# Kernel tuning notes

Hardware: AMD Instinct MI355X
Metric: run time of the kernel (lower is better)

## Reference

```python
import jax, jax.numpy as jnp
import numpy as np

B = 8192          # batch_size = len(embedds)
D = 512           # ll_p['num_channels'][-1]
C = 100           # n_classes
N_LAB = 4096      # int(B * plb), plb = 0.5
MAX_ITER = 30     # gtg_i
TOL = 1e-3        # gtg_t
ENT_EPS = 1e-20


def _mlp(x, W1, b1, W2, b2, W3, b3, Wc, bc):
    h = jax.nn.relu(x @ W1 + b1)
    h = jax.nn.relu(h @ W2 + b2)
    h = jax.nn.relu(h @ W3 + b3)
    return (h @ Wc + bc)[:, 0]  # squeeze -> [B]


def _entropy(X):
    # per-row Shannon entropy (bits), as in ALGTG utils
    return -jnp.sum(X * jnp.log2(X + ENT_EPS), axis=1)


def _gtg_entropy_hist(embedds, labels):
    # get_A: cos_sim -> zero diagonal -> clamp [0,1] -> 'mean' threshold -> 'diversity' (1-A)
    n = jnp.maximum(jnp.linalg.norm(embedds, axis=-1, keepdims=True), 1e-12)
    E = embedds / n
    A = E @ E.T                                   # [B,B]
    A = A * (1.0 - jnp.eye(B, dtype=A.dtype))     # fill_diagonal_(0)
    A = jnp.clip(A, 0.0, 1.0)
    A = jnp.where(A < jnp.mean(A), 0.0, A)        # AM_threshold_strategy == 'mean'
    A = 1.0 - A                                   # AM_strategy == 'diversity'

    # get_X: labeled rows one-hot, unlabeled rows uniform 1/C
    lab = jnp.arange(B) < N_LAB
    X0 = jnp.where(lab[:, None],
                   jax.nn.one_hot(labels, C, dtype=jnp.float32),
                   jnp.full((B, C), 1.0 / C, jnp.float32))
    hist0 = jnp.zeros((B, MAX_ITER), jnp.float32)
    unlab = ~lab

    def cond(s):
        _X, _h, i, err = s
        return (err > TOL) & (i < MAX_ITER)

    def body(s):
        X, hist, i, _err = s
        Xn = X * (A @ X)                          # replicator dynamics step
        Xn = Xn / jnp.sum(Xn, axis=1, keepdims=True)
        ent = _entropy(Xn)
        hist = hist.at[:, i].set(jnp.where(unlab, ent, 0.0))
        return (Xn, hist, i + 1, jnp.linalg.norm(Xn - X))

    init = (X0, hist0, jnp.array(0, jnp.int32), jnp.array(jnp.inf, jnp.float32))
    _, hist, _, _ = jax.lax.while_loop(cond, body, init)
    return hist


def setup_inputs() -> dict:
    key = jax.random.key(0)
    ks = jax.random.split(key, 11)
    d2, d4, d8 = D // 2, D // 4, D // 8

    def lin(k, fi, fo):
        return jax.random.normal(k, (fi, fo), jnp.float32) / np.float32(np.sqrt(fi))

    return {
        'features': jax.random.normal(ks[0], (B, 64), jnp.float32),
        'embedds': jax.random.normal(ks[1], (B, D), jnp.float32),
        'labels': jax.random.randint(ks[2], (B,), 0, C),
        'W1': lin(ks[3], D, d2), 'b1': jnp.zeros((d2,), jnp.float32),
        'W2': lin(ks[4], d2, d4), 'b2': jnp.zeros((d4,), jnp.float32),
        'W3': lin(ks[5], d4, d8), 'b3': jnp.zeros((d8,), jnp.float32),
        'Wc': lin(ks[6], d8, 1), 'bc': jnp.zeros((1,), jnp.float32),
    }


def reference(features, embedds, labels, W1, b1, W2, b2, W3, b3, Wc, bc):
    y_pred = _mlp(embedds, W1, b1, W2, b2, W3, b3, Wc, bc)        # [B]
    hist = _gtg_entropy_hist(embedds, labels)                      # [B, MAX_ITER]
    y_true = jnp.mean(hist, axis=1)                                # ent_strategy == 'mean'
    labeled_mask = jnp.arange(B) < N_LAB                           # bool [B]
    return (y_pred, y_true, labeled_mask)
```

## Files before the change

kernel.cpp:

```cpp
#include <hip/hip_runtime.h>
#include <hip/hip_bf16.h>
#include <math.h>

namespace {
constexpr int BROWS = 8192;
constexpr int NLAB  = 4096;
constexpr int NUNL  = 4096;
constexpr int CREAL = 100;
constexpr int CPAD  = 112;
constexpr int DIM   = 512;
constexpr int MAXIT = 30;

constexpr size_t MiB = 1ull << 20;
constexpr size_t OFF_S    = 0;
constexpr size_t OFF_AU   = 64 * MiB;
constexpr size_t OFF_EB   = 96 * MiB;
constexpr size_t OFF_XT0  = 96 * MiB;
constexpr size_t OFF_XT1  = 98 * MiB;
constexpr size_t OFF_XU   = 100 * MiB;
constexpr size_t OFF_PL   = 102 * MiB;
constexpr size_t OFF_HIST = 104 * MiB;
constexpr size_t OFF_ERR  = 104 * MiB + 16384;
constexpr size_t OFF_MS   = 104 * MiB + 16768;
constexpr size_t OFF_RN   = 104 * MiB + 32768;
constexpr size_t MEMSET_LEN = 20480;
}

typedef __attribute__((ext_vector_type(8))) short short8;
typedef __attribute__((ext_vector_type(4))) float floatx4;

__device__ inline ushort f2bf(float f) {
  __hip_bfloat16 h = __float2bfloat16(f);
  union { __hip_bfloat16 b; ushort u; } c; c.b = h; return c.u;
}
__device__ inline float bf2f(ushort u) {
  union { ushort u; __hip_bfloat16 b; } c; c.u = u;
  return __bfloat162float(c.b);
}
__device__ inline short8 ntload_s8(const ushort* p) {
  return __builtin_nontemporal_load((const short8*)p);
}

__global__ __launch_bounds__(64) void k_prep(const float* __restrict__ emb,
                                             ushort* __restrict__ Eb,
                                             float* __restrict__ rn) {
  int row = blockIdx.x, l = threadIdx.x;
  const float4* e4 = (const float4*)(emb + (size_t)row * DIM);
  float4 a = e4[2 * l], b = e4[2 * l + 1];
  float f[8] = {a.x, a.y, a.z, a.w, b.x, b.y, b.z, b.w};
  float s = 0.f;
#pragma unroll
  for (int q = 0; q < 8; q++) s += f[q] * f[q];
#pragma unroll
  for (int m = 1; m < 64; m <<= 1) s += __shfl_xor(s, m);
  if (l == 0) rn[row] = 1.0f / fmaxf(sqrtf(s), 1e-12f);
  union { short8 v; ushort u[8]; } o;
#pragma unroll
  for (int q = 0; q < 8; q++) o.u[q] = f2bf(f[q]);
  *(short8*)(Eb + (size_t)row * DIM + l * 8) = o.v;
}

__global__ __launch_bounds__(256) void k_initX(ushort* __restrict__ X0,
                                               ushort* __restrict__ X1,
                                               float* __restrict__ Xu,
                                               const int* __restrict__ labels) {
  int j = blockIdx.x * 256 + threadIdx.x;
  int c = blockIdx.y;
  float v;
  if (j < NLAB) v = (labels[j] == c) ? 1.0f : 0.0f;
  else          v = (c < CREAL) ? 0.01f : 0.0f;
  ushort b = f2bf(v);
  X0[(size_t)c * BROWS + j] = b;
  X1[(size_t)c * BROWS + j] = b;
  if (j >= NLAB) Xu[(size_t)(j - NLAB) * CPAD + c] = (c < CREAL) ? 0.01f : 0.0f;
}

__global__ __launch_bounds__(256) void k_mlp(const float* __restrict__ emb,
                                             const float* __restrict__ W1, const float* __restrict__ b1,
                                             const float* __restrict__ W2, const float* __restrict__ b2,
                                             const float* __restrict__ W3, const float* __restrict__ b3,
                                             const float* __restrict__ Wc, const float* __restrict__ bc,
                                             float* __restrict__ out) {
  __shared__ float xs[4][512];
  __shared__ float h1[4][256];
  __shared__ float h2[4][128];
  __shared__ float h3[4][64];
  int t = threadIdx.x;
  int r0 = blockIdx.x * 4;
  {
    const float4* src = (const float4*)(emb + (size_t)r0 * DIM);
    float4* dst = (float4*)&xs[0][0];
    dst[t] = src[t];
    dst[t + 256] = src[t + 256];
  }
  __syncthreads();
  {
    float a0 = 0.f, a1 = 0.f, a2 = 0.f, a3 = 0.f;
    for (int k = 0; k < 512; k++) {
      float w = W1[k * 256 + t];
      a0 = fmaf(xs[0][k], w, a0);
      a1 = fmaf(xs[1][k], w, a1);
      a2 = fmaf(xs[2][k], w, a2);
      a3 = fmaf(xs[3][k], w, a3);
    }
    float bb = b1[t];
    h1[0][t] = fmaxf(a0 + bb, 0.f);
    h1[1][t] = fmaxf(a1 + bb, 0.f);
    h1[2][t] = fmaxf(a2 + bb, 0.f);
    h1[3][t] = fmaxf(a3 + bb, 0.f);
  }
  __syncthreads();
  {
    int c = t & 127, rb = (t >> 7) * 2;
    float a0 = 0.f, a1 = 0.f;
    for (int k = 0; k < 256; k++) {
      float w = W2[k * 128 + c];
      a0 = fmaf(h1[rb][k], w, a0);
      a1 = fmaf(h1[rb + 1][k], w, a1);
    }
    float bb = b2[c];
    h2[rb][c] = fmaxf(a0 + bb, 0.f);
    h2[rb + 1][c] = fmaxf(a1 + bb, 0.f);
  }
  __syncthreads();
  {
    int c = t & 63, r = t >> 6;
    float a = 0.f;
    for (int k = 0; k < 128; k++) a = fmaf(h2[r][k], W3[k * 64 + c], a);
    h3[r][c] = fmaxf(a + b3[c], 0.f);
  }
  __syncthreads();
  {
    int r = t >> 6, l = t & 63;
    float v = h3[r][l] * Wc[l];
#pragma unroll
    for (int m = 32; m; m >>= 1) v += __shfl_down(v, m);
    if (l == 0) out[r0 + r] = v + bc[0];
  }
}

__global__ __launch_bounds__(256) void k_simM(const ushort* __restrict__ Eb,
                                              const float* __restrict__ rn,
                                              ushort* __restrict__ S,
                                              double* __restrict__ meansum) {
  int x = blockIdx.x, y = blockIdx.y;
  if (x < 32 && y > x) return;
  __shared__ ushort Ei[128 * 40];
  __shared__ ushort Ej[128 * 40];
  __shared__ float redbuf[4];

  int t = threadIdx.x;
  int w = t >> 6, lane = t & 63;
  int m = lane & 15, g = lane >> 4;
  int ib = (w >> 1) * 64, jb = (w & 1) * 64;
  int i0 = x * 128, j0 = y * 128;

  floatx4 acc[4][4];
#pragma unroll
  for (int a = 0; a < 4; a++)
#pragma unroll
    for (int b = 0; b < 4; b++) acc[a][b] = (floatx4)0.0f;

  int lrow = t >> 1, lhalf = (t & 1) * 16;
  for (int kt = 0; kt < DIM; kt += 32) {
    __syncthreads();
    {
      const ushort* gi = Eb + (size_t)(i0 + lrow) * DIM + kt + lhalf;
      const ushort* gj = Eb + (size_t)(j0 + lrow) * DIM + kt + lhalf;
      int o = lrow * 40 + lhalf;
      *(short8*)&Ei[o]     = *(const short8*)gi;
      *(short8*)&Ei[o + 8] = *(const short8*)(gi + 8);
      *(short8*)&Ej[o]     = *(const short8*)gj;
      *(short8*)&Ej[o + 8] = *(const short8*)(gj + 8);
    }
    __syncthreads();

    short8 ah[4], bh[4];
#pragma unroll
    for (int rt = 0; rt < 4; rt++) ah[rt] = *(const short8*)&Ei[(ib + rt * 16 + m) * 40 + g * 8];
#pragma unroll
    for (int ct = 0; ct < 4; ct++) bh[ct] = *(const short8*)&Ej[(jb + ct * 16 + m) * 40 + g * 8];
#pragma unroll
    for (int rt = 0; rt < 4; rt++)
#pragma unroll
      for (int ct = 0; ct < 4; ct++)
        acc[rt][ct] = __builtin_amdgcn_mfma_f32_16x16x32_bf16(ah[rt], bh[ct], acc[rt][ct], 0, 0, 0);
  }

  bool dostore = (x >= 32);
  bool isdiag  = (x == y);
  float weight = (x < 32) ? (isdiag ? 1.0f : 2.0f) : ((y < 32) ? 2.0f : 1.0f);
  float lsum = 0.f;
#pragma unroll
  for (int rt = 0; rt < 4; rt++) {
    int gi0 = i0 + ib + rt * 16 + g * 4;
    float4 rni = *(const float4*)(rn + gi0);
#pragma unroll
    for (int ct = 0; ct < 4; ct++) {
      int gj = j0 + jb + ct * 16 + m;
      float rnj = rn[gj];
#pragma unroll
      for (int r = 0; r < 4; r++) {
        int gi = gi0 + r;
        float rv = (r == 0) ? rni.x : (r == 1) ? rni.y : (r == 2) ? rni.z : rni.w;
        float s = acc[rt][ct][r] * rv * rnj;
        if (isdiag && gi == gj) s = 0.f;
        s = fminf(fmaxf(s, 0.f), 1.f);
        lsum += s;
        if (dostore) S[(size_t)(gi - NLAB) * BROWS + gj] = f2bf(s);
      }
    }
  }
  lsum *= weight;
#pragma unroll
  for (int d = 1; d < 64; d <<= 1) lsum += __shfl_xor(lsum, d);
  if (lane == 0) redbuf[w] = lsum;
  __syncthreads();
  if (t == 0) atomicAdd(meansum, (double)(redbuf[0] + redbuf[1] + redbuf[2] + redbuf[3]));
}

__global__ __launch_bounds__(1024, 4) void k_iter(const ushort* __restrict__ S,
                                                  ushort* __restrict__ Au,
                                                  const ushort* __restrict__ XTr,
                                                  ushort* __restrict__ XTw,
                                                  float* __restrict__ Xu,
                                                  float* __restrict__ Plab,
                                                  float* __restrict__ hist,
                                                  float* __restrict__ errsq,
                                                  const double* __restrict__ ms,
                                                  int it) {
  if (it > 0 && errsq[it - 1] <= 1e-6f) return;
  __shared__ float part[8][16 * 113];
  __shared__ float Pbuf[16 * 114];
  __shared__ float dsqbuf[16];
  ushort* xbuf = (ushort*)&part[0][0];
  int t = threadIdx.x;
  int w = t >> 6, lane = t & 63;
  int m = lane & 15, g = lane >> 4;
  int r0 = blockIdx.x * 16;

  float2 xo = make_float2(0.f, 0.f);
  if (lane < 56) xo = *(const float2*)(Xu + (size_t)(r0 + w) * CPAD + lane * 2);
  float pl_pre[2] = {0.f, 0.f};
  if (it > 0) {
#pragma unroll
    for (int q = 0; q < 2; q++) {
      int idx = t + q * 1024;
      if (idx < 16 * CPAD)
        pl_pre[q] = Plab[(size_t)(r0 + idx / CPAD) * CPAD + idx % CPAD];
    }
  }

  floatx4 acc[7];
#pragma unroll
  for (int c = 0; c < 7; c++) acc[c] = (floatx4)0.0f;

  if (it == 0) {
    float mean = (float)(ms[0] * (1.0 / ((double)BROWS * (double)BROWS)));
    int kw = w * 512;
    for (int ks = 0; ks < 16; ks++) {
      int kk = kw + ks * 32;
      size_t so = (size_t)(r0 + m) * BROWS + kk + g * 8;
      short8 a = ntload_s8(S + so);
      union { short8 v; ushort u[8]; } ua; ua.v = a;
#pragma unroll
      for (int e = 0; e < 8; e++) {
        float s = bf2f(ua.u[e]);
        float av = (s < mean) ? 1.0f : 1.0f - s;
        ua.u[e] = f2bf(av);
      }
      a = ua.v;
      if (w >= 8)
        *(short8*)(Au + (size_t)(r0 + m) * NUNL + (kk - NLAB) + g * 8) = a;
#pragma unroll
      for (int ct = 0; ct < 7; ct++) {
        short8 b = *(const short8*)(XTr + (size_t)(ct * 16 + m) * BROWS + kk + g * 8);
        acc[ct] = __builtin_amdgcn_mfma_f32_16x16x32_bf16(a, b, acc[ct], 0, 0, 0);
      }
    }
  } else {
    int kw = w * 256;
    size_t abase = (size_t)(r0 + m) * NUNL + kw + g * 8;
    size_t bbase = (size_t)m * BROWS + NLAB + kw + g * 8;
    for (int ks = 0; ks < 8; ks++) {
      short8 a = ntload_s8(Au + abase + ks * 32);
#pragma unroll
      for (int ct = 0; ct < 7; ct++) {
        short8 b = *(const short8*)(XTr + bbase + (size_t)ct * 16 * BROWS + ks * 32);
        acc[ct] = __builtin_amdgcn_mfma_f32_16x16x32_bf16(a, b, acc[ct], 0, 0, 0);
      }
    }
  }

  if (w < 8) {
#pragma unroll
    for (int ct = 0; ct < 7; ct++)
#pragma unroll
      for (int r = 0; r < 4; r++)
        part[w][(g * 4 + r) * 113 + ct * 16 + m] = acc[ct][r];
  }
  __syncthreads();
  float sA[2] = {0.f, 0.f}, sB[2] = {0.f, 0.f};
#pragma unroll
  for (int q = 0; q < 2; q++) {
    int idx = t + q * 1024;
    if (idx < 16 * CPAD) {
      int row = idx / CPAD, col = idx % CPAD;
      int o = row * 113 + col;
      sA[q] = ((part[0][o] + part[1][o]) + (part[2][o] + part[3][o]))
            + ((part[4][o] + part[5][o]) + (part[6][o] + part[7][o]));
    }
  }
  __syncthreads();
  if (w >= 8) {
#pragma unroll
    for (int ct = 0; ct < 7; ct++)
#pragma unroll
      for (int r = 0; r < 4; r++)
        part[w - 8][(g * 4 + r) * 113 + ct * 16 + m] = acc[ct][r];
  }
  __syncthreads();
#pragma unroll
  for (int q = 0; q < 2; q++) {
    int idx = t + q * 1024;
    if (idx < 16 * CPAD) {
      int row = idx / CPAD, col = idx % CPAD;
      int o = row * 113 + col;
      sB[q] = ((part[0][o] + part[1][o]) + (part[2][o] + part[3][o]))
            + ((part[4][o] + part[5][o]) + (part[6][o] + part[7][o]));
      float P;
      size_t go = (size_t)(r0 + row) * CPAD + col;
      if (it == 0) { Plab[go] = sA[q]; P = sA[q] + sB[q]; }
      else         { P = sA[q] + sB[q] + pl_pre[q]; }
      Pbuf[row * 114 + col] = P;
    }
  }
  __syncthreads();

  int gr = r0 + w;
  bool act = lane < 56;
  float2 p = make_float2(0.f, 0.f);
  if (act) p = *(const float2*)&Pbuf[w * 114 + lane * 2];
  float2 xn;
  xn.x = xo.x * p.x;
  xn.y = xo.y * p.y;
  float s = xn.x + xn.y;
#pragma unroll
  for (int d = 1; d < 64; d <<= 1) s += __shfl_xor(s, d);
  float inv = 1.0f / s;
  float ent = 0.f, dsq = 0.f;
  if (act) {
    xn.x *= inv; xn.y *= inv;
    ent = -(xn.x * log2f(xn.x + 1e-20f) + xn.y * log2f(xn.y + 1e-20f));
    float dx = xn.x - xo.x, dy = xn.y - xo.y;
    dsq = dx * dx + dy * dy;
    *(float2*)(Xu + (size_t)gr * CPAD + lane * 2) = xn;
    int c0 = lane * 2;
    xbuf[c0 * 18 + w]       = f2bf(xn.x);
    xbuf[(c0 + 1) * 18 + w] = f2bf(xn.y);
  }
#pragma unroll
  for (int d = 1; d < 64; d <<= 1) { ent += __shfl_xor(ent, d); dsq += __shfl_xor(dsq, d); }
  if (lane == 0) {
    hist[gr] += ent;
    dsqbuf[w] = dsq;
  }
  __syncthreads();

  if (t < CPAD * 8) {
    int c = t >> 3, jl = (t & 7) * 2;
    ushort2 v = *(const ushort2*)&xbuf[c * 18 + jl];
    *(ushort2*)(XTw + (size_t)c * BROWS + NLAB + r0 + jl) = v;
  }
  if (t == 0) {
    float ds = 0.f;
#pragma unroll
    for (int i = 0; i < 16; i++) ds += dsqbuf[i];
    atomicAdd(&errsq[it], ds);
  }
}

__global__ __launch_bounds__(256) void k_final(const float* __restrict__ hist,
                                               float* __restrict__ out) {
  int i = blockIdx.x * 256 + threadIdx.x;
  float yt = (i < NLAB) ? 0.0f : hist[i - NLAB] * (1.0f / 30.0f);
  out[BROWS + i] = yt;
  out[2 * BROWS + i] = (i < NLAB) ? 1.0f : 0.0f;
}

extern "C" void kernel_launch(void* const* d_in, const int* in_sizes, int n_in,
                              void* d_out, int out_size, void* d_ws, size_t ws_size,
                              hipStream_t stream) {
  const float* emb    = (const float*)d_in[1];
  const int*   labels = (const int*)d_in[2];
  const float* W1 = (const float*)d_in[3];
  const float* b1 = (const float*)d_in[4];
  const float* W2 = (const float*)d_in[5];
  const float* b2 = (const float*)d_in[6];
  const float* W3 = (const float*)d_in[7];
  const float* b3 = (const float*)d_in[8];
  const float* Wc = (const float*)d_in[9];
  const float* bc = (const float*)d_in[10];
  float* out = (float*)d_out;

  char* ws = (char*)d_ws;
  ushort* S    = (ushort*)(ws + OFF_S);
  ushort* Au   = (ushort*)(ws + OFF_AU);
  ushort* Eb   = (ushort*)(ws + OFF_EB);
  ushort* XT0  = (ushort*)(ws + OFF_XT0);
  ushort* XT1  = (ushort*)(ws + OFF_XT1);
  float*  Xu   = (float*)(ws + OFF_XU);
  float*  Plab = (float*)(ws + OFF_PL);
  float*  hist = (float*)(ws + OFF_HIST);
  float*  errs = (float*)(ws + OFF_ERR);
  double* ms   = (double*)(ws + OFF_MS);
  float*  rn   = (float*)(ws + OFF_RN);

  hipMemsetAsync(ws + OFF_HIST, 0, MEMSET_LEN, stream);

  k_prep<<<BROWS, 64, 0, stream>>>(emb, Eb, rn);
  k_mlp<<<BROWS / 4, 256, 0, stream>>>(emb, W1, b1, W2, b2, W3, b3, Wc, bc, out);

  { dim3 g(BROWS / 128, BROWS / 128); k_simM<<<g, 256, 0, stream>>>(Eb, rn, S, ms); }

  { dim3 g(BROWS / 256, CPAD); k_initX<<<g, 256, 0, stream>>>(XT0, XT1, Xu, labels); }

  for (int it = 0; it < MAXIT; it++) {
    const ushort* XTr = (it & 1) ? XT1 : XT0;
    ushort*       XTw = (it & 1) ? XT0 : XT1;
    k_iter<<<NUNL / 16, 1024, 0, stream>>>(S, Au, XTr, XTw, Xu, Plab, hist, errs, ms, it);
  }

  k_final<<<BROWS / 256, 256, 0, stream>>>(hist, out);
}
```

Measured before the change: 779.4 us.

## Batch 8 rows per MLP block, swizzle simM LDS, drop nontemporal loads

The MLP kernel now processes 8 rows per block instead of 4, so each weight load is reused across twice as many rows. The similarity GEMM kernel XOR-swizzles its shared-memory tile columns to reduce LDS bank conflicts on the MFMA operand reads. The iteration kernel replaces nontemporal loads of S and Au with ordinary loads, which may let the Au matrix that is reread every iteration stay in cache. Risks are higher LDS use and register pressure in the MLP, and cache pollution from the S stream.

```diff
diff --git a/kernel.cpp b/kernel.cpp
--- a/kernel.cpp
+++ b/kernel.cpp
@@ -37,9 +37,6 @@
   union { ushort u; __hip_bfloat16 b; } c; c.u = u;
   return __bfloat162float(c.b);
 }
-__device__ inline short8 ntload_s8(const ushort* p) {
-  return __builtin_nontemporal_load((const short8*)p);
-}
 
 __global__ __launch_bounds__(64) void k_prep(const float* __restrict__ emb,
                                              ushort* __restrict__ Eb,
@@ -81,61 +78,70 @@
                                              const float* __restrict__ W3, const float* __restrict__ b3,
                                              const float* __restrict__ Wc, const float* __restrict__ bc,
                                              float* __restrict__ out) {
-  __shared__ float xs[4][512];
-  __shared__ float h1[4][256];
-  __shared__ float h2[4][128];
-  __shared__ float h3[4][64];
+  __shared__ float xs[8][512];
+  __shared__ float h1[8][256];
+  __shared__ float h2[8][128];
+  __shared__ float h3[8][64];
   int t = threadIdx.x;
-  int r0 = blockIdx.x * 4;
+  int r0 = blockIdx.x * 8;
   {
     const float4* src = (const float4*)(emb + (size_t)r0 * DIM);
     float4* dst = (float4*)&xs[0][0];
-    dst[t] = src[t];
-    dst[t + 256] = src[t + 256];
+#pragma unroll
+    for (int q = 0; q < 4; q++) dst[t + q * 256] = src[t + q * 256];
   }
   __syncthreads();
   {
-    float a0 = 0.f, a1 = 0.f, a2 = 0.f, a3 = 0.f;
+    float a[8];
+#pragma unroll
+    for (int r = 0; r < 8; r++) a[r] = 0.f;
     for (int k = 0; k < 512; k++) {
-      float w = W1[k * 256 + t];
-      a0 = fmaf(xs[0][k], w, a0);
-      a1 = fmaf(xs[1][k], w, a1);
-      a2 = fmaf(xs[2][k], w, a2);
-      a3 = fmaf(xs[3][k], w, a3);
+      float wv = W1[k * 256 + t];
+#pragma unroll
+      for (int r = 0; r < 8; r++) a[r] = fmaf(xs[r][k], wv, a[r]);
     }
     float bb = b1[t];
-    h1[0][t] = fmaxf(a0 + bb, 0.f);
-    h1[1][t] = fmaxf(a1 + bb, 0.f);
-    h1[2][t] = fmaxf(a2 + bb, 0.f);
-    h1[3][t] = fmaxf(a3 + bb, 0.f);
+#pragma unroll
+    for (int r = 0; r < 8; r++) h1[r][t] = fmaxf(a[r] + bb, 0.f);
   }
   __syncthreads();
   {
-    int c = t & 127, rb = (t >> 7) * 2;
+    int c = t & 127, rb = (t >> 7) * 4;
+    float a[4];
+#pragma unroll
+    for (int r = 0; r < 4; r++) a[r] = 0.f;
+    for (int k = 0; k < 256; k++) {
+      float wv = W2[k * 128 + c];
+#pragma unroll
+      for (int r = 0; r < 4; r++) a[r] = fmaf(h1[rb + r][k], wv, a[r]);
+    }
+    float bb = b2[c];
+#pragma unroll
+    for (int r = 0; r < 4; r++) h2[rb + r][c] = fmaxf(a[r] + bb, 0.f);
+  }
+  __syncthreads();
+  {
+    int c = t & 63, rb = (t >> 6) * 2;
     float a0 = 0.f, a1 = 0.f;
-    for (int k = 0; k < 256; k++) {
-      float w = W2[k * 128 + c];
-      a0 = fmaf(h1[rb][k], w, a0);
-      a1 = fmaf(h1[rb + 1][k], w, a1);
-    }
-    float bb = b2[c];
-    h2[rb][c] = fmaxf(a0 + bb, 0.f);
-    h2[rb + 1][c] = fmaxf(a1 + bb, 0.f);
+    for (int k = 0; k < 128; k++) {
+      float wv = W3[k * 64 + c];
+      a0 = fmaf(h2[rb][k], wv, a0);
+      a1 = fmaf(h2[rb + 1][k], wv, a1);
+    }
+    h3[rb][c]     = fmaxf(a0 + b3[c], 0.f);
+    h3[rb + 1][c] = fmaxf(a1 + b3[c], 0.f);
   }
   __syncthreads();
   {
-    int c = t & 63, r = t >> 6;
-    float a = 0.f;
-    for (int k = 0; k < 128; k++) a = fmaf(h2[r][k], W3[k * 64 + c], a);
-    h3[r][c] = fmaxf(a + b3[c], 0.f);
-  }
-  __syncthreads();
-  {
-    int r = t >> 6, l = t & 63;
-    float v = h3[r][l] * Wc[l];
-#pragma unroll
-    for (int m = 32; m; m >>= 1) v += __shfl_down(v, m);
-    if (l == 0) out[r0 + r] = v + bc[0];
+    int w = t >> 6, l = t & 63;
+#pragma unroll
+    for (int rr = 0; rr < 2; rr++) {
+      int r = w * 2 + rr;
+      float v = h3[r][l] * Wc[l];
+#pragma unroll
+      for (int mm = 32; mm; mm >>= 1) v += __shfl_down(v, mm);
+      if (l == 0) out[r0 + r] = v + bc[0];
+    }
   }
 }
 
@@ -162,24 +168,34 @@
     for (int b = 0; b < 4; b++) acc[a][b] = (floatx4)0.0f;
 
   int lrow = t >> 1, lhalf = (t & 1) * 16;
+  int swz = ((lrow >> 3) & 3) << 3;
+  int sb  = lrow * 40;
+  int sc0 = lhalf ^ swz, sc1 = (lhalf + 8) ^ swz;
   for (int kt = 0; kt < DIM; kt += 32) {
     __syncthreads();
     {
       const ushort* gi = Eb + (size_t)(i0 + lrow) * DIM + kt + lhalf;
       const ushort* gj = Eb + (size_t)(j0 + lrow) * DIM + kt + lhalf;
-      int o = lrow * 40 + lhalf;
-      *(short8*)&Ei[o]     = *(const short8*)gi;
-      *(short8*)&Ei[o + 8] = *(const short8*)(gi + 8);
-      *(short8*)&Ej[o]     = *(const short8*)gj;
-      *(short8*)&Ej[o + 8] = *(const short8*)(gj + 8);
+      *(short8*)&Ei[sb + sc0] = *(const short8*)gi;
+      *(short8*)&Ei[sb + sc1] = *(const short8*)(gi + 8);
+      *(short8*)&Ej[sb + sc0] = *(const short8*)gj;
+      *(short8*)&Ej[sb + sc1] = *(const short8*)(gj + 8);
     }
     __syncthreads();
 
     short8 ah[4], bh[4];
 #pragma unroll
-    for (int rt = 0; rt < 4; rt++) ah[rt] = *(const short8*)&Ei[(ib + rt * 16 + m) * 40 + g * 8];
-#pragma unroll
-    for (int ct = 0; ct < 4; ct++) bh[ct] = *(const short8*)&Ej[(jb + ct * 16 + m) * 40 + g * 8];
+    for (int rt = 0; rt < 4; rt++) {
+      int row = ib + rt * 16 + m;
+      int rs = ((row >> 3) & 3) << 3;
+      ah[rt] = *(const short8*)&Ei[row * 40 + ((g * 8) ^ rs)];
+    }
+#pragma unroll
+    for (int ct = 0; ct < 4; ct++) {
+      int row = jb + ct * 16 + m;
+      int rs = ((row >> 3) & 3) << 3;
+      bh[ct] = *(const short8*)&Ej[row * 40 + ((g * 8) ^ rs)];
+    }
 #pragma unroll
     for (int rt = 0; rt < 4; rt++)
 #pragma unroll
@@ -261,7 +277,7 @@
     for (int ks = 0; ks < 16; ks++) {
       int kk = kw + ks * 32;
       size_t so = (size_t)(r0 + m) * BROWS + kk + g * 8;
-      short8 a = ntload_s8(S + so);
+      short8 a = *(const short8*)(S + so);
       union { short8 v; ushort u[8]; } ua; ua.v = a;
 #pragma unroll
       for (int e = 0; e < 8; e++) {
@@ -283,7 +299,7 @@
     size_t abase = (size_t)(r0 + m) * NUNL + kw + g * 8;
     size_t bbase = (size_t)m * BROWS + NLAB + kw + g * 8;
     for (int ks = 0; ks < 8; ks++) {
-      short8 a = ntload_s8(Au + abase + ks * 32);
+      short8 a = *(const short8*)(Au + abase + ks * 32);
 #pragma unroll
       for (int ct = 0; ct < 7; ct++) {
         short8 b = *(const short8*)(XTr + bbase + (size_t)ct * 16 * BROWS + ks * 32);
@@ -419,7 +435,7 @@
   hipMemsetAsync(ws + OFF_HIST, 0, MEMSET_LEN, stream);
 
   k_prep<<<BROWS, 64, 0, stream>>>(emb, Eb, rn);
-  k_mlp<<<BROWS / 4, 256, 0, stream>>>(emb, W1, b1, W2, b2, W3, b3, Wc, bc, out);
+  k_mlp<<<BROWS / 8, 256, 0, stream>>>(emb, W1, b1, W2, b2, W3, b3, Wc, bc, out);
 
   { dim3 g(BROWS / 128, BROWS / 128); k_simM<<<g, 256, 0, stream>>>(Eb, rn, S, ms); }
 
```

Result: faster. 729.4 us (-6.4%).
